# Kernel tuning notes

Hardware: AMD Instinct MI355X
Metric: run time of the kernel (lower is better)

## Reference

```python
import jax, jax.numpy as jnp
import numpy as np

N = 50000      # nodes
E = 1_600_000  # edges (avg degree 32)
G = 2000       # graphs in batch
H = 2          # attention heads
C = 64         # out_channels
IN = 64        # in_channels
NEG_SLOPE = 0.2


def setup_inputs() -> dict:
    key = jax.random.key(0)
    ks = jax.random.split(key, 6)
    x = jax.random.normal(ks[0], (N, IN), dtype=jnp.float32)
    edge_index = jax.random.randint(ks[1], (2, E), 0, N, dtype=jnp.int32)
    batch = jnp.sort(jax.random.randint(ks[2], (N,), 0, G, dtype=jnp.int32))
    # GATConv params: lin weight [H*C, IN] (glorot-ish), att vectors, bias [C]
    W = jax.random.normal(ks[3], (H * C, IN), dtype=jnp.float32) * (1.0 / np.sqrt(IN))
    att_src = jax.random.normal(ks[4], (1, H, C), dtype=jnp.float32) * 0.1
    att_dst = jax.random.normal(ks[5], (1, H, C), dtype=jnp.float32) * 0.1
    bias = jnp.zeros((C,), dtype=jnp.float32)
    return {"x": x, "edge_index": edge_index, "batch": batch,
            "W": W, "att_src": att_src, "att_dst": att_dst, "bias": bias}


def reference(x, edge_index, batch, W, att_src, att_dst, bias):
    # --- GATConv (PyG semantics: add_self_loops=True, concat=False -> head mean + bias) ---
    loops = jnp.arange(N, dtype=edge_index.dtype)
    src = jnp.concatenate([edge_index[0], loops])  # [E+N]
    dst = jnp.concatenate([edge_index[1], loops])  # [E+N]

    xp = (x @ W.T).reshape(N, H, C)                 # projected node feats [N,H,C]
    a_src = jnp.sum(xp * att_src, axis=-1)          # [N,H]
    a_dst = jnp.sum(xp * att_dst, axis=-1)          # [N,H]

    e = jax.nn.leaky_relu(a_src[src] + a_dst[dst], NEG_SLOPE)  # [E+N,H]
    # segment softmax over incoming edges of each destination node
    m = jax.ops.segment_max(e, dst, num_segments=N)            # [N,H]
    e = jnp.exp(e - m[dst])
    s = jax.ops.segment_sum(e, dst, num_segments=N)            # [N,H]
    alpha = e / s[dst]                                         # [E+N,H]

    msg = xp[src] * alpha[:, :, None]                          # [E+N,H,C]
    out = jax.ops.segment_sum(msg, dst, num_segments=N)        # [N,H,C]
    h_nodes = out.mean(axis=1) + bias                          # [N,C]

    # --- global_mean_pool ---
    sums = jax.ops.segment_sum(h_nodes, batch, num_segments=G)                     # [G,C]
    cnt = jax.ops.segment_sum(jnp.ones((N, 1), h_nodes.dtype), batch, num_segments=G)
    h_graphs = sums / jnp.maximum(cnt, 1.0)                                        # [G,C]
    return (h_nodes, h_graphs)
```

## Files before the change

kernel.cpp:

```cpp
#include <hip/hip_runtime.h>
#include <hip/hip_bf16.h>

#define H 2
#define C 64
#define IN_CH 64
#define HC (H*C)
#define NEG_SLOPE 0.2f
#define NBUCK_MAX 512
#define SBLK 512
#define CHUNK_MAX 3136
#define CAP 6144

__global__ __launch_bounds__(128) void proj_kernel(
    const float* __restrict__ x, const float* __restrict__ W,
    const float* __restrict__ att_src, const float* __restrict__ att_dst,
    const int* __restrict__ batch, __hip_bfloat16* __restrict__ xp,
    float* __restrict__ asrc, float* __restrict__ adst, int* __restrict__ cnt,
    int* __restrict__ gbeg, int N, int nbuck, int G) {
    int t = threadIdx.x;
    if (blockIdx.x == 0)
        for (int i = t; i < nbuck; i += 128) cnt[i] = 0;
    {
        int i = blockIdx.x * 128 + t;
        if (i < N) {
            int bi = batch[i];
            if (i == 0) {
                for (int g = 0; g <= bi; g++) gbeg[g] = 0;
            } else {
                int bp = batch[i - 1];
                for (int g = bp + 1; g <= bi; g++) gbeg[g] = i;
            }
            if (i == N - 1)
                for (int g = bi + 1; g <= G; g++) gbeg[g] = N;
        }
    }
    float w[64];
    const float4* wr = reinterpret_cast<const float4*>(W + (size_t)t * IN_CH);
#pragma unroll
    for (int q = 0; q < 16; q++) {
        float4 v = wr[q];
        w[4 * q] = v.x; w[4 * q + 1] = v.y; w[4 * q + 2] = v.z; w[4 * q + 3] = v.w;
    }
    float a_s = att_src[t], a_d = att_dst[t];
    int lane = t & 63, head = t >> 6;
    for (int n = blockIdx.x; n < N; n += gridDim.x) {
        const float* xr = x + (size_t)n * IN_CH;
        float acc = 0.f;
#pragma unroll
        for (int k = 0; k < 64; k++) acc = fmaf(w[k], xr[k], acc);
        xp[(size_t)n * HC + t] = __float2bfloat16(acc);
        float as = acc * a_s, ad = acc * a_d;
#pragma unroll
        for (int d = 32; d > 0; d >>= 1) {
            as += __shfl_xor(as, d, 64);
            ad += __shfl_xor(ad, d, 64);
        }
        if (lane == 0) {
            asrc[(size_t)n * H + head] = as;
            adst[(size_t)n * H + head] = ad;
        }
    }
}

__global__ __launch_bounds__(256) void scatter_kernel(
    const int* __restrict__ edge, int* __restrict__ cnt,
    int* __restrict__ staged, int N, int E) {
    const int tid = threadIdx.x, bid = blockIdx.x;
    const int nbuck = (N + 127) >> 7;
    const int chunkE = (E + SBLK - 1) / SBLK;
    const int* srcE = edge;
    const int* dstE = edge + E;
    __shared__ int2 eds[CHUNK_MAX];
    __shared__ int lh[NBUCK_MAX], bse[NBUCK_MAX], lcur[NBUCK_MAX];
    for (int i = tid; i < nbuck; i += 256) { lh[i] = 0; lcur[i] = 0; }
    __syncthreads();
    int beg = bid * chunkE, end = min(beg + chunkE, E);
    int m = end - beg;
    for (int i = tid; i < m; i += 256) {
        int s = srcE[beg + i], d = dstE[beg + i];
        eds[i] = make_int2(s, d);
        atomicAdd(&lh[d >> 7], 1);
    }
    __syncthreads();
    for (int i = tid; i < nbuck; i += 256)
        bse[i] = atomicAdd(&cnt[i], lh[i]);
    __syncthreads();
    for (int i = tid; i < m; i += 256) {
        int2 e = eds[i];
        int b = e.y >> 7;
        int l = atomicAdd(&lcur[b], 1);
        staged[(size_t)b * CAP + bse[b] + l] = e.x | ((e.y & 127) << 20);
    }
}

__global__ __launch_bounds__(512) void bucket_csr_kernel(
    const int* __restrict__ staged, const int* __restrict__ cnt,
    int* __restrict__ off, int* __restrict__ csr, int N, int nbuck) {
    int b = blockIdx.x, t = threadIdx.x;
    __shared__ int bse[512], rs[512], lh[128], sh[128], cur[128];
    {
        int v = (t < nbuck) ? cnt[t] : 0;
        bse[t] = v; rs[t] = v;
        __syncthreads();
        for (int d = 1; d < 512; d <<= 1) {
            int u = (t >= d) ? bse[t - d] : 0;
            __syncthreads();
            bse[t] += u;
            __syncthreads();
        }
        bse[t] -= rs[t];
        __syncthreads();
    }
    int base = bse[b], size = rs[b];
    const int* st = staged + (size_t)b * CAP;
    if (t < 128) lh[t] = 0;
    __syncthreads();
    for (int i = t; i < size; i += 512)
        atomicAdd(&lh[st[i] >> 20], 1);
    __syncthreads();
    int v = (t < 128) ? lh[t] : 0;
    if (t < 128) sh[t] = v;
    __syncthreads();
    for (int d = 1; d < 128; d <<= 1) {
        int u = (t >= d && t < 128) ? sh[t - d] : 0;
        __syncthreads();
        if (t < 128) sh[t] += u;
        __syncthreads();
    }
    if (t < 128) {
        int ex = sh[t] - v;
        int nd = b * 128 + t;
        if (nd < N) off[nd] = base + ex;
        if (nd == N - 1) off[N] = base + size;
        cur[t] = base + ex;
    }
    __syncthreads();
    for (int i = t; i < size; i += 512) {
        int e = st[i];
        int pos = atomicAdd(&cur[e >> 20], 1);
        csr[pos] = e & 0xFFFFF;
    }
}

template<int NB>
__device__ __forceinline__ void gfma(const uint* __restrict__ xpw,
                                     const int* __restrict__ si,
                                     const float* __restrict__ swl,
                                     uint laneoff, float& accx, float& accy) {
    const char* xb = reinterpret_cast<const char*>(xpw);
    uint bu[NB];
#pragma unroll
    for (int j = 0; j < NB; j++) {
        uint boff = (uint)si[j] + laneoff;
        bu[j] = *reinterpret_cast<const uint*>(xb + boff);
    }
#pragma unroll
    for (int j = 0; j < NB; j++) {
        float w = swl[2 * j];
        accx = fmaf(w, __uint_as_float(bu[j] << 16), accx);
        accy = fmaf(w, __uint_as_float(bu[j] & 0xffff0000u), accy);
    }
}

__global__ __launch_bounds__(256, 8) void aggregate_kernel(
    const __hip_bfloat16* __restrict__ xp, const float* __restrict__ asrc,
    const float* __restrict__ adst, const int* __restrict__ off,
    const int* __restrict__ csr, const float* __restrict__ bias,
    float* __restrict__ out, int N) {
    __shared__ int sidx[4][32];
    __shared__ float swf[4][64];
    int wid = threadIdx.x >> 6;
    int n = blockIdx.x * 4 + wid;
    if (n >= N) return;
    int lane = threadIdx.x & 63;
    int cl = lane & 31;
    int hsel = lane >> 5;
    int* si = sidx[wid];
    float* swl = swf[wid] + hsel;
    int o0 = off[n];
    int deg = off[n + 1] - o0;
    float adh = adst[2 * n + hsel];
    float es = asrc[2 * n + hsel] + adh;
    es = (es > 0.f) ? es : NEG_SLOPE * es;
    float wself = __expf(es);
    float ssum = (cl == 0) ? wself : 0.f;

    const uint* xpw = reinterpret_cast<const uint*>(xp);
    uint laneoff = (uint)lane * 4u;
    float accx, accy;
    {
        uint u = xpw[(size_t)n * 64 + lane];
        accx = wself * __uint_as_float(u << 16);
        accy = wself * __uint_as_float(u & 0xffff0000u);
    }

    for (int base = 0; base < deg; base += 32) {
        int i = base + cl;
        int idx = 0;
        float w = 0.f;
        if (i < deg) {
            idx = csr[o0 + i];
            float t = asrc[2 * idx + hsel] + adh;
            t = (t > 0.f) ? t : NEG_SLOPE * t;
            w = __expf(t);
        }
        ssum += w;
        if (!hsel) si[cl] = idx << 8;
        swl[2 * cl] = w;
        int nb = min(deg - base, 32);
        if (nb > 16) gfma<32>(xpw, si, swl, laneoff, accx, accy);
        else         gfma<16>(xpw, si, swl, laneoff, accx, accy);
    }
#pragma unroll
    for (int d = 16; d > 0; d >>= 1) ssum += __shfl_xor(ssum, d, 64);
    float inv = 1.f / ssum;
    accx *= inv;
    accy *= inv;
    float ox = 0.5f * (accx + __shfl_xor(accx, 32, 64));
    float oy = 0.5f * (accy + __shfl_xor(accy, 32, 64));
    if (lane < 32) {
        float vx = ox + bias[2 * cl];
        float vy = oy + bias[2 * cl + 1];
        *reinterpret_cast<float2*>(out + (size_t)n * C + 2 * cl) = make_float2(vx, vy);
    }
}

__global__ __launch_bounds__(256) void pool_kernel(const float* __restrict__ hn,
                                                   const int* __restrict__ gbeg,
                                                   float* __restrict__ outG, int G) {
    int g = blockIdx.x;
    int c = threadIdx.x & 63, r = threadIdx.x >> 6;
    int beg = gbeg[g], end = gbeg[g + 1];
    float s = 0.f;
    for (int n = beg + r; n < end; n += 4) s += hn[(size_t)n * C + c];
    __shared__ float red[256];
    red[threadIdx.x] = s;
    __syncthreads();
    if (r == 0) {
        float tot = red[c] + red[64 + c] + red[128 + c] + red[192 + c];
        outG[(size_t)g * C + c] = tot / fmaxf((float)(end - beg), 1.f);
    }
}

extern "C" void kernel_launch(void* const* d_in, const int* in_sizes, int n_in,
                              void* d_out, int out_size, void* d_ws, size_t ws_size,
                              hipStream_t stream) {
    const float* x       = (const float*)d_in[0];
    const int*   edge    = (const int*)d_in[1];
    const int*   batch   = (const int*)d_in[2];
    const float* W       = (const float*)d_in[3];
    const float* att_src = (const float*)d_in[4];
    const float* att_dst = (const float*)d_in[5];
    const float* bias    = (const float*)d_in[6];

    int N = in_sizes[0] / IN_CH;
    int E = in_sizes[1] / 2;
    int G = out_size / C - N;
    int nbuck = (N + 127) >> 7;

    char* p = (char*)d_ws;
    auto alloc = [&](size_t bytes) {
        char* r = p;
        p += (bytes + 255) & ~(size_t)255;
        return r;
    };
    __hip_bfloat16* xp = (__hip_bfloat16*)alloc((size_t)N * HC * 2);
    float* asrc    = (float*)alloc((size_t)N * H * 4);
    float* adst    = (float*)alloc((size_t)N * H * 4);
    int*   cnt     = (int*)alloc((size_t)nbuck * 4);
    int*   off     = (int*)alloc((size_t)(N + 1) * 4);
    int*   staged  = (int*)alloc((size_t)nbuck * CAP * 4);
    int*   csr     = (int*)alloc((size_t)E * 4);
    int*   gbeg    = (int*)alloc((size_t)(G + 1) * 4);

    proj_kernel<<<2048, 128, 0, stream>>>(x, W, att_src, att_dst, batch, xp, asrc, adst,
                                          cnt, gbeg, N, nbuck, G);
    scatter_kernel<<<SBLK, 256, 0, stream>>>(edge, cnt, staged, N, E);
    bucket_csr_kernel<<<nbuck, 512, 0, stream>>>(staged, cnt, off, csr, N, nbuck);
    aggregate_kernel<<<(N + 3) / 4, 256, 0, stream>>>(xp, asrc, adst, off, csr, bias,
                                                      (float*)d_out, N);
    pool_kernel<<<G, 256, 0, stream>>>((const float*)d_out, gbeg,
                                       (float*)d_out + (size_t)N * C, G);
}
```

Baseline: 212.4 us.

## Replace bucketed two-pass CSR build with global degree-count and atomic fill

```diff
diff --git a/kernel.cpp b/kernel.cpp
--- a/kernel.cpp
+++ b/kernel.cpp
@@ -7,19 +7,25 @@
 #define HC (H*C)
 #define NEG_SLOPE 0.2f
 #define NBUCK_MAX 512
-#define SBLK 512
-#define CHUNK_MAX 3136
-#define CAP 6144
+
+__global__ __launch_bounds__(256) void zero_kernel(int* __restrict__ deg, int N) {
+    int i = blockIdx.x * 256 + threadIdx.x;
+    if (i < N) deg[i] = 0;
+}
 
 __global__ __launch_bounds__(128) void proj_kernel(
     const float* __restrict__ x, const float* __restrict__ W,
     const float* __restrict__ att_src, const float* __restrict__ att_dst,
-    const int* __restrict__ batch, __hip_bfloat16* __restrict__ xp,
-    float* __restrict__ asrc, float* __restrict__ adst, int* __restrict__ cnt,
-    int* __restrict__ gbeg, int N, int nbuck, int G) {
+    const int* __restrict__ batch, const int* __restrict__ edge,
+    __hip_bfloat16* __restrict__ xp,
+    float* __restrict__ asrc, float* __restrict__ adst, int* __restrict__ deg,
+    int* __restrict__ gbeg, int N, int E, int G) {
     int t = threadIdx.x;
-    if (blockIdx.x == 0)
-        for (int i = t; i < nbuck; i += 128) cnt[i] = 0;
+    {
+        const int* dstE = edge + E;
+        for (int e = blockIdx.x * 128 + t; e < E; e += gridDim.x * 128)
+            atomicAdd(&deg[dstE[e]], 1);
+    }
     {
         int i = blockIdx.x * 128 + t;
         if (i < N) {
@@ -62,44 +68,28 @@
     }
 }
 
-__global__ __launch_bounds__(256) void scatter_kernel(
-    const int* __restrict__ edge, int* __restrict__ cnt,
-    int* __restrict__ staged, int N, int E) {
-    const int tid = threadIdx.x, bid = blockIdx.x;
-    const int nbuck = (N + 127) >> 7;
-    const int chunkE = (E + SBLK - 1) / SBLK;
-    const int* srcE = edge;
-    const int* dstE = edge + E;
-    __shared__ int2 eds[CHUNK_MAX];
-    __shared__ int lh[NBUCK_MAX], bse[NBUCK_MAX], lcur[NBUCK_MAX];
-    for (int i = tid; i < nbuck; i += 256) { lh[i] = 0; lcur[i] = 0; }
+__global__ __launch_bounds__(128) void chunk_sum_kernel(const int* __restrict__ deg,
+                                                        int* __restrict__ bsum, int N) {
+    int b = blockIdx.x, t = threadIdx.x;
+    int nd = b * 128 + t;
+    int v = (nd < N) ? deg[nd] : 0;
+#pragma unroll
+    for (int d = 32; d > 0; d >>= 1) v += __shfl_xor(v, d, 64);
+    __shared__ int s2[2];
+    if ((t & 63) == 0) s2[t >> 6] = v;
     __syncthreads();
-    int beg = bid * chunkE, end = min(beg + chunkE, E);
-    int m = end - beg;
-    for (int i = tid; i < m; i += 256) {
-        int s = srcE[beg + i], d = dstE[beg + i];
-        eds[i] = make_int2(s, d);
-        atomicAdd(&lh[d >> 7], 1);
-    }
-    __syncthreads();
-    for (int i = tid; i < nbuck; i += 256)
-        bse[i] = atomicAdd(&cnt[i], lh[i]);
-    __syncthreads();
-    for (int i = tid; i < m; i += 256) {
-        int2 e = eds[i];
-        int b = e.y >> 7;
-        int l = atomicAdd(&lcur[b], 1);
-        staged[(size_t)b * CAP + bse[b] + l] = e.x | ((e.y & 127) << 20);
-    }
-}
-
-__global__ __launch_bounds__(512) void bucket_csr_kernel(
-    const int* __restrict__ staged, const int* __restrict__ cnt,
-    int* __restrict__ off, int* __restrict__ csr, int N, int nbuck) {
+    if (t == 0) bsum[b] = s2[0] + s2[1];
+}
+
+__global__ __launch_bounds__(512) void prep_kernel(const int* __restrict__ deg,
+                                                   const int* __restrict__ bsum,
+                                                   int* __restrict__ off,
+                                                   int* __restrict__ cur,
+                                                   int N, int nbuck) {
     int b = blockIdx.x, t = threadIdx.x;
-    __shared__ int bse[512], rs[512], lh[128], sh[128], cur[128];
-    {
-        int v = (t < nbuck) ? cnt[t] : 0;
+    __shared__ int bse[512], rs[512], sh[128];
+    {
+        int v = (t < nbuck) ? bsum[t] : 0;
         bse[t] = v; rs[t] = v;
         __syncthreads();
         for (int d = 1; d < 512; d <<= 1) {
@@ -108,18 +98,11 @@
             bse[t] += u;
             __syncthreads();
         }
-        bse[t] -= rs[t];
-        __syncthreads();
-    }
-    int base = bse[b], size = rs[b];
-    const int* st = staged + (size_t)b * CAP;
-    if (t < 128) lh[t] = 0;
-    __syncthreads();
-    for (int i = t; i < size; i += 512)
-        atomicAdd(&lh[st[i] >> 20], 1);
-    __syncthreads();
-    int v = (t < 128) ? lh[t] : 0;
-    if (t < 128) sh[t] = v;
+    }
+    int base = bse[b] - rs[b];
+    int nd = b * 128 + t;
+    int dv = (t < 128 && nd < N) ? deg[nd] : 0;
+    if (t < 128) sh[t] = dv;
     __syncthreads();
     for (int d = 1; d < 128; d <<= 1) {
         int u = (t >= d && t < 128) ? sh[t - d] : 0;
@@ -128,17 +111,21 @@
         __syncthreads();
     }
     if (t < 128) {
-        int ex = sh[t] - v;
-        int nd = b * 128 + t;
-        if (nd < N) off[nd] = base + ex;
-        if (nd == N - 1) off[N] = base + size;
-        cur[t] = base + ex;
-    }
-    __syncthreads();
-    for (int i = t; i < size; i += 512) {
-        int e = st[i];
-        int pos = atomicAdd(&cur[e >> 20], 1);
-        csr[pos] = e & 0xFFFFF;
+        int ex = sh[t] - dv;
+        if (nd < N) { off[nd] = base + ex; cur[nd] = base + ex; }
+        if (nd == N - 1) off[N] = base + ex + dv;
+    }
+}
+
+__global__ __launch_bounds__(256) void fill_kernel(const int* __restrict__ edge,
+                                                   int* __restrict__ cur,
+                                                   int* __restrict__ csr, int E) {
+    const int* srcE = edge;
+    const int* dstE = edge + E;
+    for (int i = blockIdx.x * 256 + threadIdx.x; i < E; i += gridDim.x * 256) {
+        int d = dstE[i], s = srcE[i];
+        int pos = atomicAdd(&cur[d], 1);
+        csr[pos] = s;
     }
 }
 
@@ -162,7 +149,7 @@
     }
 }
 
-__global__ __launch_bounds__(256, 8) void aggregate_kernel(
+__global__ __launch_bounds__(256, 4) void aggregate_kernel(
     const __hip_bfloat16* __restrict__ xp, const float* __restrict__ asrc,
     const float* __restrict__ adst, const int* __restrict__ off,
     const int* __restrict__ csr, const float* __restrict__ bias,
@@ -267,16 +254,19 @@
     __hip_bfloat16* xp = (__hip_bfloat16*)alloc((size_t)N * HC * 2);
     float* asrc    = (float*)alloc((size_t)N * H * 4);
     float* adst    = (float*)alloc((size_t)N * H * 4);
-    int*   cnt     = (int*)alloc((size_t)nbuck * 4);
+    int*   deg     = (int*)alloc((size_t)N * 4);
+    int*   cur     = (int*)alloc((size_t)N * 4);
+    int*   bsum    = (int*)alloc((size_t)NBUCK_MAX * 4);
     int*   off     = (int*)alloc((size_t)(N + 1) * 4);
-    int*   staged  = (int*)alloc((size_t)nbuck * CAP * 4);
     int*   csr     = (int*)alloc((size_t)E * 4);
     int*   gbeg    = (int*)alloc((size_t)(G + 1) * 4);
 
-    proj_kernel<<<2048, 128, 0, stream>>>(x, W, att_src, att_dst, batch, xp, asrc, adst,
-                                          cnt, gbeg, N, nbuck, G);
-    scatter_kernel<<<SBLK, 256, 0, stream>>>(edge, cnt, staged, N, E);
-    bucket_csr_kernel<<<nbuck, 512, 0, stream>>>(staged, cnt, off, csr, N, nbuck);
+    zero_kernel<<<(N + 255) / 256, 256, 0, stream>>>(deg, N);
+    proj_kernel<<<2048, 128, 0, stream>>>(x, W, att_src, att_dst, batch, edge, xp,
+                                          asrc, adst, deg, gbeg, N, E, G);
+    chunk_sum_kernel<<<nbuck, 128, 0, stream>>>(deg, bsum, N);
+    prep_kernel<<<nbuck, 512, 0, stream>>>(deg, bsum, off, cur, N, nbuck);
+    fill_kernel<<<1024, 256, 0, stream>>>(edge, cur, csr, E);
     aggregate_kernel<<<(N + 3) / 4, 256, 0, stream>>>(xp, asrc, adst, off, csr, bias,
                                                       (float*)d_out, N);
     pool_kernel<<<G, 256, 0, stream>>>((const float*)d_out, gbeg,
```

Result: slower. 363.3 us (+71.1%).
